# Kernel optimization log

Hardware: AMD Instinct MI355X
Metric: run time of the kernel (lower is better)

The kernel has to match this reference:

```python
import jax, jax.numpy as jnp
import numpy as np


def setup_inputs() -> dict:
    key = jax.random.key(0)
    k1, k2 = jax.random.split(key)
    src_map = jax.random.normal(k1, (8, 256, 48, 48), dtype=jnp.float32)
    dst_map = jax.random.normal(k2, (8, 256, 48, 48), dtype=jnp.float32)
    return {"src_map": src_map, "dst_map": dst_map}


def reference(src_map, dst_map):
    # src_map: [B, C, H, W] -> flatten spatial to S = H*W
    B, C, H, W = src_map.shape
    src_flat = src_map.reshape(B, C, H * W)                 # [B, C, S]
    # L2-normalize along channel dim (torch.norm default: 2-norm, no eps)
    src = src_flat / jnp.linalg.norm(src_flat, axis=1, keepdims=True)
    dst = dst_map / jnp.linalg.norm(dst_map, axis=1, keepdims=True)  # [B, C, Y, X]
    # cosine correlation volume: for each src pixel s, dot with every dst pixel
    gcm = jnp.einsum('bcs,bcyx->bsyx', src, dst)            # [B, S, Y, X]
    # torch.max(gcm, 0) == ReLU clamp
    return jnp.maximum(gcm, 0.0)
```

## Files before the change

kernel.cpp:

```cpp
#include <hip/hip_runtime.h>
#include <hip/hip_bf16.h>

#define B_DIM 8
#define C_DIM 256
#define S_DIM 2304


typedef __attribute__((ext_vector_type(8))) short short8;
typedef __attribute__((ext_vector_type(4))) float floatx4;

__global__ __launch_bounds__(256) void norm_transpose_kernel(
    const float* __restrict__ src, const float* __restrict__ dst,
    __hip_bfloat16* __restrict__ srcT, __hip_bfloat16* __restrict__ dstT) {
    const int s0 = blockIdx.x * 64;
    const int b  = blockIdx.y;
    const float* in = (blockIdx.z == 0 ? src : dst) + (size_t)b * C_DIM * S_DIM;
    __hip_bfloat16* out = (blockIdx.z == 0 ? srcT : dstT) + (size_t)b * S_DIM * C_DIM;

    __shared__ __align__(16) __hip_bfloat16 tile[64][C_DIM];
    __shared__ float red[4][64];
    __shared__ float invn[64];

    const int t  = threadIdx.x;
    const int l  = t & 63;
    const int wv = t >> 6;

    float ss = 0.f;
#pragma unroll 2
    for (int q = 0; q < 8; ++q) {
        int oct = 4 * q + wv;
        union { short8 v; __hip_bfloat16 h[8]; } o;
#pragma unroll
        for (int j = 0; j < 8; ++j) {
            float v = in[(size_t)(oct * 8 + j) * S_DIM + s0 + l];
            ss += v * v;
            o.h[j] = __float2bfloat16(v);
        }
        *(short8*)((char*)&tile[l][0] + ((oct * 16) ^ ((l & 7) << 4))) = o.v;
    }
    red[wv][l] = ss;
    __syncthreads();
    if (t < 64) invn[t] = rsqrtf(red[0][t] + red[1][t] + red[2][t] + red[3][t]);
    __syncthreads();

#pragma unroll
    for (int it = 0; it < 8; ++it) {
        int gidx = it * 256 + t;
        int fm   = gidx & 15;
        int cg   = (gidx >> 4) & 31;
        int sg   = gidx >> 9;
        int srow = sg * 16 + fm;
        float inv = invn[srow];
        union { short8 v; __hip_bfloat16 h[8]; } u, o;
        u.v = *(const short8*)((const char*)&tile[srow][0]
                               + ((cg * 16) ^ ((srow & 7) << 4)));
#pragma unroll
        for (int j = 0; j < 8; ++j)
            o.h[j] = __float2bfloat16(__bfloat162float(u.h[j]) * inv);
        *(short8*)&out[(size_t)((s0 >> 4) + sg) * 4096 + cg * 128 + fm * 8] = o.v;
    }
}

__global__ __launch_bounds__(256, 3) void gemm_relu_kernel(
    const __hip_bfloat16* __restrict__ At, const __hip_bfloat16* __restrict__ Bt,
    float* __restrict__ out) {
    const int id = blockIdx.x;
    const int b  = id & 7;
    const int q  = id >> 3;
    const int m0 = (q % 18) * 128;
    const int n0 = (q / 18) * 128;

    __shared__ __align__(16) float Cs[64 * 132];

    const int t    = threadIdx.x;
    const int lane = t & 63;
    const int wv   = t >> 6;

    const int fm = lane & 15;
    const int wr = (wv >> 1) << 6;
    const int wc = (wv & 1) << 6;
    const int rq = (lane >> 4) << 2;

    const __hip_bfloat16* pA = At + (size_t)b * S_DIM * C_DIM
                             + (size_t)((m0 + wr) >> 4) * 4096 + lane * 8;
    const __hip_bfloat16* pB = Bt + (size_t)b * S_DIM * C_DIM
                             + (size_t)((n0 + wc) >> 4) * 4096 + lane * 8;

    floatx4 acc[4][4] = {};
    short8 a0[4], b0[4], a1[4], b1[4];

#pragma unroll
    for (int i = 0; i < 4; ++i) {
        a0[i] = *(const short8*)(pA + i * 4096);
        b0[i] = *(const short8*)(pB + i * 4096);
    }

#pragma unroll
    for (int ki = 0; ki < 8; ki += 2) {
#pragma unroll
        for (int i = 0; i < 4; ++i) {
            a1[i] = *(const short8*)(pA + i * 4096 + (ki + 1) * 512);
            b1[i] = *(const short8*)(pB + i * 4096 + (ki + 1) * 512);
        }
        __builtin_amdgcn_s_setprio(1);
#pragma unroll
        for (int i = 0; i < 4; ++i)
#pragma unroll
            for (int j = 0; j < 4; ++j)
                acc[i][j] = __builtin_amdgcn_mfma_f32_16x16x32_bf16(a0[i], b0[j], acc[i][j], 0, 0, 0);
        __builtin_amdgcn_s_setprio(0);

        if (ki + 2 < 8) {
#pragma unroll
            for (int i = 0; i < 4; ++i) {
                a0[i] = *(const short8*)(pA + i * 4096 + (ki + 2) * 512);
                b0[i] = *(const short8*)(pB + i * 4096 + (ki + 2) * 512);
            }
        }
        __builtin_amdgcn_s_setprio(1);
#pragma unroll
        for (int i = 0; i < 4; ++i)
#pragma unroll
            for (int j = 0; j < 4; ++j)
                acc[i][j] = __builtin_amdgcn_mfma_f32_16x16x32_bf16(a1[i], b1[j], acc[i][j], 0, 0, 0);
        __builtin_amdgcn_s_setprio(0);
    }

    float* Cp = out + (size_t)b * S_DIM * S_DIM;
#pragma unroll
    for (int p = 0; p < 2; ++p) {
        __syncthreads();
#pragma unroll
        for (int i2 = 0; i2 < 2; ++i2) {
            int i = 2 * p + i2;
            int slot = (wr >> 1) + i2 * 16 + rq;
#pragma unroll
            for (int j = 0; j < 4; ++j) {
                int col = wc + j * 16 + fm;
#pragma unroll
                for (int r = 0; r < 4; ++r)
                    Cs[(slot + r) * 132 + col] = fmaxf(acc[i][j][r], 0.f);
            }
        }
        __syncthreads();
#pragma unroll
        for (int it = 0; it < 8; ++it) {
            int idx  = it * 256 + t;
            int srow = idx >> 5;
            int c4   = (idx & 31) << 2;
            floatx4 v = *(const floatx4*)&Cs[srow * 132 + c4];
            int lrow = 32 * p + (srow & 31) + ((srow >> 5) << 6);
            __builtin_nontemporal_store(
                v, (floatx4*)&Cp[(size_t)(m0 + lrow) * S_DIM + n0 + c4]);
        }
    }
}

extern "C" void kernel_launch(void* const* d_in, const int* in_sizes, int n_in,
                              void* d_out, int out_size, void* d_ws, size_t ws_size,
                              hipStream_t stream) {
    const float* src = (const float*)d_in[0];
    const float* dst = (const float*)d_in[1];
    float* out = (float*)d_out;

    __hip_bfloat16* srcT = (__hip_bfloat16*)d_ws;
    __hip_bfloat16* dstT = srcT + (size_t)B_DIM * S_DIM * C_DIM;

    dim3 g1(S_DIM / 64, B_DIM, 2);
    norm_transpose_kernel<<<g1, 256, 0, stream>>>(src, dst, srcT, dstT);

    gemm_relu_kernel<<<dim3(B_DIM * 18 * 18), 256, 0, stream>>>(srcT, dstT, out);
}
```

Measured before the change: 206.1 us.

## Enlarge GEMM tile to 256x256 with 512 threads and LDS-staged double-buffered operands

The GEMM block tile grows from 128x128 with 256 threads to 256x256 with 512 threads. A and B K-slices are now staged through double-buffered shared memory and shared across waves, where before each wave loaded its operand fragments straight from global memory. The aim is fewer redundant global operand loads and more reuse per loaded byte. In exchange the grid shrinks to 648 blocks, which can leave the GPU poorly balanced, and each K step now needs a barrier. The epilogue is restructured to write 64-row strips through the reused shared buffer.

```diff
diff --git a/kernel.cpp b/kernel.cpp
--- a/kernel.cpp
+++ b/kernel.cpp
@@ -8,6 +8,10 @@
 
 typedef __attribute__((ext_vector_type(8))) short short8;
 typedef __attribute__((ext_vector_type(4))) float floatx4;
+
+__device__ __forceinline__ void barrier_lgkm() {
+    asm volatile("s_waitcnt lgkmcnt(0)\n\ts_barrier" ::: "memory");
+}
 
 __global__ __launch_bounds__(256) void norm_transpose_kernel(
     const float* __restrict__ src, const float* __restrict__ dst,
@@ -61,97 +65,117 @@
     }
 }
 
-__global__ __launch_bounds__(256, 3) void gemm_relu_kernel(
+__global__ __launch_bounds__(512, 2) void gemm_relu_kernel(
     const __hip_bfloat16* __restrict__ At, const __hip_bfloat16* __restrict__ Bt,
     float* __restrict__ out) {
     const int id = blockIdx.x;
     const int b  = id & 7;
     const int q  = id >> 3;
-    const int m0 = (q % 18) * 128;
-    const int n0 = (q / 18) * 128;
+    const int m0 = (q % 9) * 256;
+    const int n0 = (q / 9) * 256;
 
-    __shared__ __align__(16) float Cs[64 * 132];
+    __shared__ __align__(16) unsigned char smem[66560];
+    __hip_bfloat16* stg = (__hip_bfloat16*)smem;
+    float* Cs = (float*)smem;
 
     const int t    = threadIdx.x;
     const int lane = t & 63;
     const int wv   = t >> 6;
 
-    const int fm = lane & 15;
-    const int wr = (wv >> 1) << 6;
-    const int wc = (wv & 1) << 6;
-    const int rq = (lane >> 4) << 2;
+    const int fm  = lane & 15;
+    const int kq4 = lane >> 4;
+    const int rq  = kq4 << 2;
+    const int wr2 = wv >> 2;
+    const int wc2 = wv & 3;
 
-    const __hip_bfloat16* pA = At + (size_t)b * S_DIM * C_DIM
-                             + (size_t)((m0 + wr) >> 4) * 4096 + lane * 8;
-    const __hip_bfloat16* pB = Bt + (size_t)b * S_DIM * C_DIM
-                             + (size_t)((n0 + wc) >> 4) * 4096 + lane * 8;
+    const int seg0 = t >> 4;
+    const int lq   = (t & 15);
+    const int sA0g = seg0 >> 2, sA0c = seg0 & 3;
+    const int seg1 = seg0 + 32;
+    const int sA1g = seg1 >> 2, sA1c = seg1 & 3;
 
-    floatx4 acc[4][4] = {};
-    short8 a0[4], b0[4], a1[4], b1[4];
+    const __hip_bfloat16* Ab = At + (size_t)b * S_DIM * C_DIM;
+    const __hip_bfloat16* Bb = Bt + (size_t)b * S_DIM * C_DIM;
+    const __hip_bfloat16* gA0 = Ab + (size_t)((m0 >> 4) + sA0g) * 4096 + sA0c * 128 + lq * 8;
+    const __hip_bfloat16* gA1 = Ab + (size_t)((m0 >> 4) + sA1g) * 4096 + sA1c * 128 + lq * 8;
+    const __hip_bfloat16* gB0 = Bb + (size_t)((n0 >> 4) + sA0g) * 4096 + sA0c * 128 + lq * 8;
+    const __hip_bfloat16* gB1 = Bb + (size_t)((n0 >> 4) + sA1g) * 4096 + sA1c * 128 + lq * 8;
+    const int l0 = seg0 * 128 + lq * 8;
+    const int l1 = seg1 * 128 + lq * 8;
+
+    short8 rA0 = *(const short8*)gA0;
+    short8 rA1 = *(const short8*)gA1;
+    short8 rB0 = *(const short8*)gB0;
+    short8 rB1 = *(const short8*)gB1;
+
+    floatx4 acc[8][4] = {};
 
 #pragma unroll
-    for (int i = 0; i < 4; ++i) {
-        a0[i] = *(const short8*)(pA + i * 4096);
-        b0[i] = *(const short8*)(pB + i * 4096);
-    }
+    for (int ki = 0; ki < 8; ++ki) {
+        __hip_bfloat16* As = stg + (ki & 1) * 16384;
+        __hip_bfloat16* Bs = As + 8192;
 
+        *(short8*)(As + l0) = rA0;
+        *(short8*)(As + l1) = rA1;
+        *(short8*)(Bs + l0) = rB0;
+        *(short8*)(Bs + l1) = rB1;
+
+        if (ki < 7) {
+            int off = (ki + 1) * 512;
+            rA0 = *(const short8*)(gA0 + off);
+            rA1 = *(const short8*)(gA1 + off);
+            rB0 = *(const short8*)(gB0 + off);
+            rB1 = *(const short8*)(gB1 + off);
+        }
+
+        barrier_lgkm();
+
+        short8 af[8], bf[4];
 #pragma unroll
-    for (int ki = 0; ki < 8; ki += 2) {
+        for (int i = 0; i < 8; ++i)
+            af[i] = *(const short8*)&As[((wr2 * 8 + i) * 4 + kq4) * 128 + fm * 8];
 #pragma unroll
-        for (int i = 0; i < 4; ++i) {
-            a1[i] = *(const short8*)(pA + i * 4096 + (ki + 1) * 512);
-            b1[i] = *(const short8*)(pB + i * 4096 + (ki + 1) * 512);
-        }
+        for (int j = 0; j < 4; ++j)
+            bf[j] = *(const short8*)&Bs[((wc2 * 4 + j) * 4 + kq4) * 128 + fm * 8];
+
         __builtin_amdgcn_s_setprio(1);
 #pragma unroll
-        for (int i = 0; i < 4; ++i)
+        for (int i = 0; i < 8; ++i)
 #pragma unroll
             for (int j = 0; j < 4; ++j)
-                acc[i][j] = __builtin_amdgcn_mfma_f32_16x16x32_bf16(a0[i], b0[j], acc[i][j], 0, 0, 0);
-        __builtin_amdgcn_s_setprio(0);
-
-        if (ki + 2 < 8) {
-#pragma unroll
-            for (int i = 0; i < 4; ++i) {
-                a0[i] = *(const short8*)(pA + i * 4096 + (ki + 2) * 512);
-                b0[i] = *(const short8*)(pB + i * 4096 + (ki + 2) * 512);
-            }
-        }
-        __builtin_amdgcn_s_setprio(1);
-#pragma unroll
-        for (int i = 0; i < 4; ++i)
-#pragma unroll
-            for (int j = 0; j < 4; ++j)
-                acc[i][j] = __builtin_amdgcn_mfma_f32_16x16x32_bf16(a1[i], b1[j], acc[i][j], 0, 0, 0);
+                acc[i][j] = __builtin_amdgcn_mfma_f32_16x16x32_bf16(af[i], bf[j], acc[i][j], 0, 0, 0);
         __builtin_amdgcn_s_setprio(0);
     }
 
     float* Cp = out + (size_t)b * S_DIM * S_DIM;
 #pragma unroll
-    for (int p = 0; p < 2; ++p) {
+    for (int p = 0; p < 4; ++p) {
         __syncthreads();
+        if (wr2 == (p >> 1)) {
 #pragma unroll
-        for (int i2 = 0; i2 < 2; ++i2) {
-            int i = 2 * p + i2;
-            int slot = (wr >> 1) + i2 * 16 + rq;
+            for (int i2 = 0; i2 < 2; ++i2) {
 #pragma unroll
-            for (int j = 0; j < 4; ++j) {
-                int col = wc + j * 16 + fm;
+                for (int j = 0; j < 4; ++j) {
+                    int col = wc2 * 64 + j * 16 + fm;
 #pragma unroll
-                for (int r = 0; r < 4; ++r)
-                    Cs[(slot + r) * 132 + col] = fmaxf(acc[i][j][r], 0.f);
+                    for (int r = 0; r < 4; ++r) {
+                        Cs[(i2 * 16 + rq + r) * 260 + col] =
+                            fmaxf(acc[4 * (p & 1) + i2][j][r], 0.f);
+                        Cs[((i2 + 2) * 16 + rq + r) * 260 + col] =
+                            fmaxf(acc[4 * (p & 1) + i2 + 2][j][r], 0.f);
+                    }
+                }
             }
         }
         __syncthreads();
 #pragma unroll
         for (int it = 0; it < 8; ++it) {
-            int idx  = it * 256 + t;
-            int srow = idx >> 5;
-            int c4   = (idx & 31) << 2;
-            floatx4 v = *(const floatx4*)&Cs[srow * 132 + c4];
-            int lrow = 32 * p + (srow & 31) + ((srow >> 5) << 6);
+            int idx  = it * 512 + t;
+            int srow = idx >> 6;
+            int c4   = (idx & 63) << 2;
+            floatx4 v = *(const floatx4*)&Cs[srow * 260 + c4];
             __builtin_nontemporal_store(
-                v, (floatx4*)&Cp[(size_t)(m0 + lrow) * S_DIM + n0 + c4]);
+                v, (floatx4*)&Cp[(size_t)(m0 + p * 64 + srow) * S_DIM + n0 + c4]);
         }
     }
 }
@@ -169,5 +193,5 @@
     dim3 g1(S_DIM / 64, B_DIM, 2);
     norm_transpose_kernel<<<g1, 256, 0, stream>>>(src, dst, srcT, dstT);
 
-    gemm_relu_kernel<<<dim3(B_DIM * 18 * 18), 256, 0, stream>>>(srcT, dstT, out);
+    gemm_relu_kernel<<<dim3(B_DIM * 9 * 9), 512, 0, stream>>>(srcT, dstT, out);
 }
```

After: 218.9 us. 1.06x slower.
